# Kernel optimization log

Measured on AMD Instinct MI355X. Metric: run time of the kernel, lower is better.

## Reference

```python
import jax, jax.numpy as jnp
import numpy as np

INPUT_SIZE = 10000
GROUP_SIZE = 500
STEP = GROUP_SIZE // 2            # 250
OUT_PER_GROUP = 50
GROUPS = 2 * INPUT_SIZE // GROUP_SIZE - 1  # 39


def setup_inputs() -> dict:
    key = jax.random.key(0)
    k1, k2 = jax.random.split(key)
    x = jax.random.uniform(k1, (4096, INPUT_SIZE), dtype=jnp.float32)
    # torch init: uniform_(weight, 0.9, 1.1); weight shape per group is [out, in]
    W = jax.random.uniform(k2, (GROUPS, OUT_PER_GROUP, GROUP_SIZE),
                           dtype=jnp.float32, minval=0.9, maxval=1.1)
    return {"x": x, "W": W}


def reference(x, W):
    # gather overlapping windows: idx[g, k] = g*STEP + k  -> [B, GROUPS, GROUP_SIZE]
    idx = jnp.arange(GROUPS)[:, None] * STEP + jnp.arange(GROUP_SIZE)[None, :]
    xw = x[:, idx]                                   # [B, G, K]
    # per-group linear (no bias): out[b,g,o] = sum_k xw[b,g,k] * W[g,o,k]
    out = jnp.einsum('bgk,gok->bgo', xw, W)          # [B, G, O]
    return jax.nn.relu(out.reshape(x.shape[0], GROUPS * OUT_PER_GROUP))
```

## Files before the change

### kernel.cpp

```cpp
#include <hip/hip_runtime.h>
#include <hip/hip_bf16.h>


constexpr int INPUT  = 10000;
constexpr int GROUPS = 39;
constexpr int GS     = 500;
constexpr int STEP   = 250;
constexpr int OPG    = 50;
constexpr int OUTW   = GROUPS * OPG;

constexpr int BM  = 128;
constexpr int KH  = 256;
constexpr int LDB = KH + 8;

typedef __attribute__((ext_vector_type(8))) short  short8;
typedef __attribute__((ext_vector_type(4))) float  float4v;

__device__ __forceinline__ unsigned bf2pack(float a, float b) {
    union { float f; unsigned u; } x, y; x.f = a; y.f = b;
    unsigned lo = (x.u + 0x7fffu + ((x.u >> 16) & 1u)) >> 16;
    unsigned hi = (y.u + 0x7fffu + ((y.u >> 16) & 1u)) & 0xffff0000u;
    return hi | lo;
}

template<bool TAIL>
__device__ __forceinline__ short8 load_a_frag(const float* base, int koff, int kglob) {
    float2 c0 = {0.f, 0.f}, c1 = {0.f, 0.f}, c2 = {0.f, 0.f}, c3 = {0.f, 0.f};
    if (!TAIL) {
        c0 = *(const float2*)(base + koff);
        c1 = *(const float2*)(base + koff + 2);
        c2 = *(const float2*)(base + koff + 4);
        c3 = *(const float2*)(base + koff + 6);
    } else {
        if (kglob + 2 <= GS) c0 = *(const float2*)(base + koff);
        if (kglob + 4 <= GS) c1 = *(const float2*)(base + koff + 2);
        if (kglob + 6 <= GS) c2 = *(const float2*)(base + koff + 4);
        if (kglob + 8 <= GS) c3 = *(const float2*)(base + koff + 6);
    }
    union { short8 s; unsigned u[4]; } f;
    f.u[0] = bf2pack(c0.x, c0.y);
    f.u[1] = bf2pack(c1.x, c1.y);
    f.u[2] = bf2pack(c2.x, c2.y);
    f.u[3] = bf2pack(c3.x, c3.y);
    return f.s;
}

__global__ __launch_bounds__(256, 4)
void peak_binner_kernel(const float* __restrict__ x,
                        const float* __restrict__ W,
                        float* __restrict__ out, int batch)
{
    __shared__ __align__(16) short Bs[64 * LDB];

    const int g    = blockIdx.x;
    const int m0   = blockIdx.y * BM;
    const int tid  = threadIdx.x;
    const int lane = tid & 63;
    const int wave = tid >> 6;

    const int fm = lane & 15;
    const int fk = (lane >> 4) * 8;

    const long  col0 = (long)g * STEP;
    const float* Wg  = W + (size_t)g * OPG * GS;

    const float* Abase[2];
    #pragma unroll
    for (int mt = 0; mt < 2; ++mt) {
        const int row = m0 + wave * 32 + mt * 16 + fm;
        Abase[mt] = x + (size_t)row * INPUT + col0 + fk;
    }

    float4v acc[2][4];
    #pragma unroll
    for (int i = 0; i < 2; ++i)
        #pragma unroll
        for (int j = 0; j < 4; ++j)
            acc[i][j] = {0.f, 0.f, 0.f, 0.f};

    #pragma unroll
    for (int h = 0; h < 2; ++h) {
        const int k0 = h * KH;
        if (h) __syncthreads();

        for (int c = tid; c < OPG * (KH / 2); c += 256) {
            const int o  = c >> 7;
            const int kc = (c & 127) << 1;
            const int k  = k0 + kc;
            float2 v = {0.f, 0.f};
            if (k < GS) v = *(const float2*)(Wg + o * GS + k);
            *(unsigned*)&Bs[o * LDB + kc] = bf2pack(v.x, v.y);
        }
        __syncthreads();

        #pragma unroll
        for (int kk = 0; kk < KH; kk += 32) {
            short8 a[2];
            if (h == 1 && kk == KH - 32) {
                a[0] = load_a_frag<true>(Abase[0], k0 + kk, k0 + kk + fk);
                a[1] = load_a_frag<true>(Abase[1], k0 + kk, k0 + kk + fk);
            } else {
                a[0] = load_a_frag<false>(Abase[0], k0 + kk, 0);
                a[1] = load_a_frag<false>(Abase[1], k0 + kk, 0);
            }
            short8 b[4];
            #pragma unroll
            for (int nt = 0; nt < 4; ++nt)
                b[nt] = *(const short8*)&Bs[(nt * 16 + fm) * LDB + kk + fk];
            #pragma unroll
            for (int mt = 0; mt < 2; ++mt)
                #pragma unroll
                for (int nt = 0; nt < 4; ++nt)
                    acc[mt][nt] = __builtin_amdgcn_mfma_f32_16x16x32_bf16(
                        a[mt], b[nt], acc[mt][nt], 0, 0, 0);
        }
    }

    const int orow = (lane >> 4) * 4;
    const int ocol = lane & 15;
    #pragma unroll
    for (int mt = 0; mt < 2; ++mt) {
        #pragma unroll
        for (int reg = 0; reg < 4; ++reg) {
            const int row = m0 + wave * 32 + mt * 16 + orow + reg;
            if (row >= batch) continue;
            float* op = out + (size_t)row * OUTW + g * OPG;
            #pragma unroll
            for (int nt = 0; nt < 4; ++nt) {
                const int o = nt * 16 + ocol;
                if (o < OPG) op[o] = fmaxf(acc[mt][nt][reg], 0.f);
            }
        }
    }
}

extern "C" void kernel_launch(void* const* d_in, const int* in_sizes, int n_in,
                              void* d_out, int out_size, void* d_ws, size_t ws_size,
                              hipStream_t stream) {
    const float* x = (const float*)d_in[0];
    const float* W = (const float*)d_in[1];
    float* out     = (float*)d_out;

    const int batch = in_sizes[0] / INPUT;
    dim3 grid(GROUPS, (batch + BM - 1) / BM);
    peak_binner_kernel<<<grid, dim3(256), 0, stream>>>(x, W, out, batch);
}
```

Measured before the change: 302.3 us.

## Stage x and W tiles into LDS via direct global-to-LDS loads in K-chunks

```diff
diff --git a/kernel.cpp b/kernel.cpp
--- a/kernel.cpp
+++ b/kernel.cpp
@@ -10,11 +10,29 @@
 constexpr int OUTW   = GROUPS * OPG;
 
 constexpr int BM  = 128;
-constexpr int KH  = 256;
-constexpr int LDB = KH + 8;
+constexpr int BK  = 64;
+constexpr int NST = 8;
+constexpr int RCH  = 17;
+constexpr int ROWB = RCH * 16;
+constexpr int A_BYTES = BM * ROWB;
+constexpr int B_BYTES = 64 * ROWB;
 
 typedef __attribute__((ext_vector_type(8))) short  short8;
 typedef __attribute__((ext_vector_type(4))) float  float4v;
+
+typedef const __attribute__((address_space(1))) unsigned int* gptr_t;
+typedef __attribute__((address_space(3))) unsigned int*       lptr_t;
+
+__device__ __forceinline__ void gl_lds16(const void* g, void* l) {
+    __builtin_amdgcn_global_load_lds((gptr_t)(unsigned long long)g,
+                                     (lptr_t)(unsigned int)(unsigned long long)l,
+                                     16, 0, 0);
+}
+__device__ __forceinline__ void gl_lds4(const void* g, void* l) {
+    __builtin_amdgcn_global_load_lds((gptr_t)(unsigned long long)g,
+                                     (lptr_t)(unsigned int)(unsigned long long)l,
+                                     4, 0, 0);
+}
 
 __device__ __forceinline__ unsigned bf2pack(float a, float b) {
     union { float f; unsigned u; } x, y; x.f = a; y.f = b;
@@ -22,54 +40,35 @@
     unsigned hi = (y.u + 0x7fffu + ((y.u >> 16) & 1u)) & 0xffff0000u;
     return hi | lo;
 }
-
-template<bool TAIL>
-__device__ __forceinline__ short8 load_a_frag(const float* base, int koff, int kglob) {
-    float2 c0 = {0.f, 0.f}, c1 = {0.f, 0.f}, c2 = {0.f, 0.f}, c3 = {0.f, 0.f};
-    if (!TAIL) {
-        c0 = *(const float2*)(base + koff);
-        c1 = *(const float2*)(base + koff + 2);
-        c2 = *(const float2*)(base + koff + 4);
-        c3 = *(const float2*)(base + koff + 6);
-    } else {
-        if (kglob + 2 <= GS) c0 = *(const float2*)(base + koff);
-        if (kglob + 4 <= GS) c1 = *(const float2*)(base + koff + 2);
-        if (kglob + 6 <= GS) c2 = *(const float2*)(base + koff + 4);
-        if (kglob + 8 <= GS) c3 = *(const float2*)(base + koff + 6);
-    }
-    union { short8 s; unsigned u[4]; } f;
-    f.u[0] = bf2pack(c0.x, c0.y);
-    f.u[1] = bf2pack(c1.x, c1.y);
-    f.u[2] = bf2pack(c2.x, c2.y);
-    f.u[3] = bf2pack(c3.x, c3.y);
-    return f.s;
+__device__ __forceinline__ short8 pack8(float4 lo, float4 hi) {
+    union { short8 s; unsigned u[4]; } r;
+    r.u[0] = bf2pack(lo.x, lo.y);
+    r.u[1] = bf2pack(lo.z, lo.w);
+    r.u[2] = bf2pack(hi.x, hi.y);
+    r.u[3] = bf2pack(hi.z, hi.w);
+    return r.s;
 }
 
-__global__ __launch_bounds__(256, 4)
+__global__ __launch_bounds__(256, 3)
 void peak_binner_kernel(const float* __restrict__ x,
                         const float* __restrict__ W,
                         float* __restrict__ out, int batch)
 {
-    __shared__ __align__(16) short Bs[64 * LDB];
+    __shared__ __align__(16) char lds[A_BYTES + B_BYTES];
+    char* Abuf = lds;
+    char* Bbuf = lds + A_BYTES;
 
     const int g    = blockIdx.x;
     const int m0   = blockIdx.y * BM;
     const int tid  = threadIdx.x;
     const int lane = tid & 63;
     const int wave = tid >> 6;
+    const int fm   = lane & 15;
+    const int l4   = lane >> 4;
 
-    const int fm = lane & 15;
-    const int fk = (lane >> 4) * 8;
-
-    const long  col0 = (long)g * STEP;
-    const float* Wg  = W + (size_t)g * OPG * GS;
-
-    const float* Abase[2];
-    #pragma unroll
-    for (int mt = 0; mt < 2; ++mt) {
-        const int row = m0 + wave * 32 + mt * 16 + fm;
-        Abase[mt] = x + (size_t)row * INPUT + col0 + fk;
-    }
+    const float* xg = x + (size_t)g * STEP;
+    const float* Wg = W + (size_t)g * OPG * GS;
+    const bool aligned16 = ((g & 1) == 0);
 
     float4v acc[2][4];
     #pragma unroll
@@ -78,35 +77,71 @@
         for (int j = 0; j < 4; ++j)
             acc[i][j] = {0.f, 0.f, 0.f, 0.f};
 
-    #pragma unroll
-    for (int h = 0; h < 2; ++h) {
-        const int k0 = h * KH;
-        if (h) __syncthreads();
+    for (int stage = 0; stage < NST; ++stage) {
+        const int kb = stage * BK;
+        __syncthreads();
 
-        for (int c = tid; c < OPG * (KH / 2); c += 256) {
-            const int o  = c >> 7;
-            const int kc = (c & 127) << 1;
-            const int k  = k0 + kc;
-            float2 v = {0.f, 0.f};
-            if (k < GS) v = *(const float2*)(Wg + o * GS + k);
-            *(unsigned*)&Bs[o * LDB + kc] = bf2pack(v.x, v.y);
+        if (aligned16) {
+            const int cmax = (GS - 1 - kb) >> 2;
+            for (int j = wave; j < (A_BYTES / 1024); j += 4) {
+                const int f   = j * 64 + lane;
+                const int row = f / RCH;
+                int c = f - row * RCH;
+                c = min(c, cmax);
+                const int grow = min(m0 + row, batch - 1);
+                gl_lds16(xg + (size_t)grow * INPUT + kb + 4 * c, Abuf + j * 1024);
+            }
+        } else {
+            const int qmax = GS - 1 - kb;
+            for (int j = wave; j < (A_BYTES / 256); j += 4) {
+                const int d   = j * 64 + lane;
+                const int row = d / (RCH * 4);
+                int q = d - row * (RCH * 4);
+                q = min(q, qmax);
+                const int grow = min(m0 + row, batch - 1);
+                gl_lds4(xg + (size_t)grow * INPUT + kb + q, Abuf + j * 256);
+            }
+        }
+        {
+            const int cmax = (GS - 4 - kb) >> 2;
+            for (int j = wave; j < (B_BYTES / 1024); j += 4) {
+                const int f   = j * 64 + lane;
+                const int row = f / RCH;
+                int c = f - row * RCH;
+                c = min(c, cmax);
+                const int ro = min(row, OPG - 1);
+                gl_lds16(Wg + ro * GS + kb + 4 * c, Bbuf + j * 1024);
+            }
         }
         __syncthreads();
 
+        if (stage == NST - 1) {
+            if (tid < 192) {
+                const int row = tid / 3;
+                const int c   = 13 + (tid - row * 3);
+                *(float4*)(Bbuf + row * ROWB + c * 16) = float4{0.f, 0.f, 0.f, 0.f};
+            }
+            __syncthreads();
+        }
+
         #pragma unroll
-        for (int kk = 0; kk < KH; kk += 32) {
-            short8 a[2];
-            if (h == 1 && kk == KH - 32) {
-                a[0] = load_a_frag<true>(Abase[0], k0 + kk, k0 + kk + fk);
-                a[1] = load_a_frag<true>(Abase[1], k0 + kk, k0 + kk + fk);
-            } else {
-                a[0] = load_a_frag<false>(Abase[0], k0 + kk, 0);
-                a[1] = load_a_frag<false>(Abase[1], k0 + kk, 0);
+        for (int kk = 0; kk < 2; ++kk) {
+            const int pb = (kk * 8 + l4 * 2) * 16;
+            short8 a[2], b[4];
+            #pragma unroll
+            for (int mt = 0; mt < 2; ++mt) {
+                const char* base = Abuf + (wave * 32 + mt * 16 + fm) * ROWB + pb;
+                float4 lo = *(const float4*)(base);
+                float4 hi = *(const float4*)(base + 16);
+                a[mt] = pack8(lo, hi);
             }
-            short8 b[4];
             #pragma unroll
-            for (int nt = 0; nt < 4; ++nt)
-                b[nt] = *(const short8*)&Bs[(nt * 16 + fm) * LDB + kk + fk];
+            for (int nt = 0; nt < 4; ++nt) {
+                const char* base = Bbuf + (nt * 16 + fm) * ROWB + pb;
+                float4 lo = *(const float4*)(base);
+                float4 hi = *(const float4*)(base + 16);
+                b[nt] = pack8(lo, hi);
+            }
             #pragma unroll
             for (int mt = 0; mt < 2; ++mt)
                 #pragma unroll
```

Result: no change. 297.9 us (-1.5%).

## Pre-convert W to padded bf16 and stage coalesced x tiles in LDS

Applied to the files above, without the earlier changes.

```diff
diff --git a/kernel.cpp b/kernel.cpp
--- a/kernel.cpp
+++ b/kernel.cpp
@@ -7,11 +7,12 @@
 constexpr int GS     = 500;
 constexpr int STEP   = 250;
 constexpr int OPG    = 50;
-constexpr int OUTW   = GROUPS * OPG;
+constexpr int OUTW   = 1950;
+constexpr int KP     = 512;
+constexpr int BM     = 32;
+constexpr int LDA    = KP + 8;
 
-constexpr int BM  = 128;
-constexpr int KH  = 256;
-constexpr int LDB = KH + 8;
+__device__ __hip_bfloat16 Wb[GROUPS * OPG * KP];
 
 typedef __attribute__((ext_vector_type(8))) short  short8;
 typedef __attribute__((ext_vector_type(4))) float  float4v;
@@ -23,114 +24,73 @@
     return hi | lo;
 }
 
-template<bool TAIL>
-__device__ __forceinline__ short8 load_a_frag(const float* base, int koff, int kglob) {
-    float2 c0 = {0.f, 0.f}, c1 = {0.f, 0.f}, c2 = {0.f, 0.f}, c3 = {0.f, 0.f};
-    if (!TAIL) {
-        c0 = *(const float2*)(base + koff);
-        c1 = *(const float2*)(base + koff + 2);
-        c2 = *(const float2*)(base + koff + 4);
-        c3 = *(const float2*)(base + koff + 6);
-    } else {
-        if (kglob + 2 <= GS) c0 = *(const float2*)(base + koff);
-        if (kglob + 4 <= GS) c1 = *(const float2*)(base + koff + 2);
-        if (kglob + 6 <= GS) c2 = *(const float2*)(base + koff + 4);
-        if (kglob + 8 <= GS) c3 = *(const float2*)(base + koff + 6);
-    }
-    union { short8 s; unsigned u[4]; } f;
-    f.u[0] = bf2pack(c0.x, c0.y);
-    f.u[1] = bf2pack(c1.x, c1.y);
-    f.u[2] = bf2pack(c2.x, c2.y);
-    f.u[3] = bf2pack(c3.x, c3.y);
-    return f.s;
+__global__ void prep_w(const float* __restrict__ W) {
+    const int slot = blockIdx.x * 256 + threadIdx.x;
+    if (slot >= GROUPS * OPG * (KP / 2)) return;
+    const int go = slot / (KP / 2);
+    const int k  = (slot - go * (KP / 2)) * 2;
+    float2 v = {0.f, 0.f};
+    if (k < GS) v = *(const float2*)(W + (size_t)go * GS + k);
+    ((unsigned*)Wb)[slot] = bf2pack(v.x, v.y);
 }
 
 __global__ __launch_bounds__(256, 4)
 void peak_binner_kernel(const float* __restrict__ x,
-                        const float* __restrict__ W,
                         float* __restrict__ out, int batch)
 {
-    __shared__ __align__(16) short Bs[64 * LDB];
+    __shared__ __align__(16) short As[BM * LDA];
 
     const int g    = blockIdx.x;
     const int m0   = blockIdx.y * BM;
     const int tid  = threadIdx.x;
     const int lane = tid & 63;
     const int wave = tid >> 6;
+    const int fm   = lane & 15;
+    const int l4   = lane >> 4;
+    const int nb   = (wave == 3) ? 34 : wave * 16;
 
-    const int fm = lane & 15;
-    const int fk = (lane >> 4) * 8;
-
-    const long  col0 = (long)g * STEP;
-    const float* Wg  = W + (size_t)g * OPG * GS;
-
-    const float* Abase[2];
+    const bool lvalid = (tid < STEP);
     #pragma unroll
-    for (int mt = 0; mt < 2; ++mt) {
-        const int row = m0 + wave * 32 + mt * 16 + fm;
-        Abase[mt] = x + (size_t)row * INPUT + col0 + fk;
-    }
-
-    float4v acc[2][4];
-    #pragma unroll
-    for (int i = 0; i < 2; ++i)
+    for (int bb = 0; bb < 4; ++bb) {
+        float2 v[8];
         #pragma unroll
-        for (int j = 0; j < 4; ++j)
-            acc[i][j] = {0.f, 0.f, 0.f, 0.f};
-
-    #pragma unroll
-    for (int h = 0; h < 2; ++h) {
-        const int k0 = h * KH;
-        if (h) __syncthreads();
-
-        for (int c = tid; c < OPG * (KH / 2); c += 256) {
-            const int o  = c >> 7;
-            const int kc = (c & 127) << 1;
-            const int k  = k0 + kc;
-            float2 v = {0.f, 0.f};
-            if (k < GS) v = *(const float2*)(Wg + o * GS + k);
-            *(unsigned*)&Bs[o * LDB + kc] = bf2pack(v.x, v.y);
+        for (int j = 0; j < 8; ++j) {
+            const int it = bb * 8 + j;
+            const int gr = min(m0 + it, batch - 1);
+            v[j] = lvalid ? *(const float2*)(x + (size_t)gr * INPUT + g * STEP + 2 * tid)
+                          : float2{0.f, 0.f};
         }
-        __syncthreads();
-
         #pragma unroll
-        for (int kk = 0; kk < KH; kk += 32) {
-            short8 a[2];
-            if (h == 1 && kk == KH - 32) {
-                a[0] = load_a_frag<true>(Abase[0], k0 + kk, k0 + kk + fk);
-                a[1] = load_a_frag<true>(Abase[1], k0 + kk, k0 + kk + fk);
-            } else {
-                a[0] = load_a_frag<false>(Abase[0], k0 + kk, 0);
-                a[1] = load_a_frag<false>(Abase[1], k0 + kk, 0);
-            }
-            short8 b[4];
-            #pragma unroll
-            for (int nt = 0; nt < 4; ++nt)
-                b[nt] = *(const short8*)&Bs[(nt * 16 + fm) * LDB + kk + fk];
-            #pragma unroll
-            for (int mt = 0; mt < 2; ++mt)
-                #pragma unroll
-                for (int nt = 0; nt < 4; ++nt)
-                    acc[mt][nt] = __builtin_amdgcn_mfma_f32_16x16x32_bf16(
-                        a[mt], b[nt], acc[mt][nt], 0, 0, 0);
+        for (int j = 0; j < 8; ++j) {
+            const int it = bb * 8 + j;
+            *(unsigned*)&As[it * LDA + 2 * tid] = bf2pack(v[j].x, v[j].y);
         }
     }
 
-    const int orow = (lane >> 4) * 4;
-    const int ocol = lane & 15;
+    float4v acc[2] = {{0,0,0,0},{0,0,0,0}};
+    const __hip_bfloat16* wp = Wb + ((size_t)g * OPG + nb + fm) * KP + l4 * 8;
+
+    __syncthreads();
+
     #pragma unroll
-    for (int mt = 0; mt < 2; ++mt) {
+    for (int kk = 0; kk < 16; ++kk) {
+        const short8 b  = *(const short8*)(wp + kk * 32);
+        const short8 a0 = *(const short8*)&As[fm        * LDA + kk * 32 + l4 * 8];
+        const short8 a1 = *(const short8*)&As[(16 + fm) * LDA + kk * 32 + l4 * 8];
+        acc[0] = __builtin_amdgcn_mfma_f32_16x16x32_bf16(a0, b, acc[0], 0, 0, 0);
+        acc[1] = __builtin_amdgcn_mfma_f32_16x16x32_bf16(a1, b, acc[1], 0, 0, 0);
+    }
+
+    if (wave < 3 || fm >= 14) {
+        const int col = g * OPG + nb + fm;
         #pragma unroll
-        for (int reg = 0; reg < 4; ++reg) {
-            const int row = m0 + wave * 32 + mt * 16 + orow + reg;
-            if (row >= batch) continue;
-            float* op = out + (size_t)row * OUTW + g * OPG;
+        for (int mt = 0; mt < 2; ++mt)
             #pragma unroll
-            for (int nt = 0; nt < 4; ++nt) {
-                const int o = nt * 16 + ocol;
-                if (o < OPG) op[o] = fmaxf(acc[mt][nt][reg], 0.f);
+            for (int reg = 0; reg < 4; ++reg) {
+                const int row = m0 + mt * 16 + l4 * 4 + reg;
+                if (row < batch)
+                    out[(size_t)row * OUTW + col] = fmaxf(acc[mt][reg], 0.f);
             }
-        }
     }
 }
 
@@ -142,6 +102,10 @@
     float* out     = (float*)d_out;
 
     const int batch = in_sizes[0] / INPUT;
+
+    const int slots = GROUPS * OPG * (KP / 2);
+    prep_w<<<(slots + 255) / 256, 256, 0, stream>>>(W);
+
     dim3 grid(GROUPS, (batch + BM - 1) / BM);
-    peak_binner_kernel<<<grid, dim3(256), 0, stream>>>(x, W, out, batch);
+    peak_binner_kernel<<<grid, dim3(256), 0, stream>>>(x, out, batch);
 }
```

After: 280.8 us. 7.1% less time.
